# Performance work log

Hardware: AMD Instinct MI355X
Metric: run time of the kernel (lower is better)

Reference implementation:

```python
import jax, jax.numpy as jnp
import numpy as np

B, L, D = 8, 256, 256  # batch, max sentence length, channel_in == channel_out


def setup_inputs() -> dict:
    key = jax.random.key(0)
    k1, k2, k3, k4, k5, k6 = jax.random.split(key, 6)
    queries = jax.random.normal(k1, (B, L, D), dtype=jnp.float32)
    wordlens = jax.random.randint(k2, (B,), 1, L, dtype=jnp.int32)
    syntactic_dep = jax.random.randint(k3, (B, L, L), 0, 2, dtype=jnp.int32)
    # w_wc[0]: Linear(2D -> D, no bias); split its weight into the h_i and h_j halves.
    s1 = 1.0 / np.sqrt(2 * D)
    Wa = jax.random.normal(k4, (D, D), dtype=jnp.float32) * s1
    Wb = jax.random.normal(jax.random.fold_in(k4, 1), (D, D), dtype=jnp.float32) * s1
    # w_wc[3]: Linear(D -> 1, no bias)
    w2 = jax.random.normal(k5, (D,), dtype=jnp.float32) * (1.0 / np.sqrt(D))
    # wd: Linear(D -> D, no bias)
    Wd = jax.random.normal(k6, (D, D), dtype=jnp.float32) * (1.0 / np.sqrt(D))
    return {"queries": queries, "wordlens": wordlens, "syntactic_dep": syntactic_dep,
            "Wa": Wa, "Wb": Wb, "w2": w2, "Wd": Wd}


def reference(queries, wordlens, syntactic_dep, Wa, Wb, w2, Wd):
    # queries: [B, L, D]; syntactic_dep: [B, L, L] (nonzero => edge i->j)
    mask = syntactic_dep > 0
    # Edge score t_ij = w2 . relu(Wa h_i + Wb h_j)  (dropout is identity at eval)
    A = jnp.einsum('bid,cd->bic', queries, Wa)   # [B, L, C]
    Bm = jnp.einsum('bjd,cd->bjc', queries, Wb)  # [B, L, C]
    pre = jax.nn.relu(A[:, :, None, :] + Bm[:, None, :, :])  # [B, L, L, C]
    t = jnp.einsum('bijc,c->bij', pre, w2)       # [B, L, L]
    # T initialized to -100 everywhere, edge positions get t (exactly as original)
    T = jnp.where(mask, t, jnp.float32(-100.0))
    beta = jax.nn.softmax(T, axis=-1)            # softmax over j (dim=1 of [L, L])
    w = beta * mask.astype(beta.dtype)           # zero out non-edges after softmax
    hj = jnp.einsum('bjd,cd->bjc', queries, Wd)  # wd(h_j), [B, L, C]
    agg = jnp.einsum('bij,bjc->bic', w, hj)      # weighted neighbor sum
    output = jax.nn.relu(queries + agg)
    # skip=False, so no extra residual add
    return (output, wordlens, syntactic_dep)
```

## Files before the change

### kernel.cpp

```cpp
#include <hip/hip_runtime.h>

#define NB 8
#define LL 256
#define DD 256

typedef __attribute__((ext_vector_type(8))) short short8v;
typedef __attribute__((ext_vector_type(4))) float f32x4;

__device__ __forceinline__ uint f2bf2(float lo, float hi) {
  uint a = __float_as_uint(lo), b = __float_as_uint(hi);
  uint ra = (a + 0x7FFFu + ((a >> 16) & 1u)) >> 16;
  uint rb = (b + 0x7FFFu + ((b >> 16) & 1u)) & 0xFFFF0000u;
  return ra | rb;
}

__global__ __launch_bounds__(256) void gemm3_mfma(
    const float* __restrict__ Q, const float* __restrict__ Wa,
    const float* __restrict__ Wb, const float* __restrict__ Wd,
    float* __restrict__ A, float* __restrict__ Bm, float* __restrict__ Hj) {
  const int mt = blockIdx.x, nt = blockIdx.y, z = blockIdx.z;
  const float* __restrict__ W = (z == 0) ? Wa : (z == 1) ? Wb : Wd;
  float* __restrict__ Out = (z == 0) ? A : (z == 1) ? Bm : Hj;

  __shared__ __align__(16) ushort Qs[64][32];
  __shared__ __align__(16) ushort Ws[64][32];

  const int tid = threadIdx.x;
  const int m0 = mt * 64, n0 = nt * 64;
  const int srow = tid >> 2, skc = (tid & 3) * 8;
  const int w = tid >> 6, lane = tid & 63;
  const int wm = w >> 1, wn = w & 1;
  const int fr = lane & 15, fk = (lane >> 4) * 8;

  f32x4 acc[2][2] = {};
  for (int k0 = 0; k0 < DD; k0 += 32) {
    {
      const float* src = &Q[(size_t)(m0 + srow) * DD + k0 + skc];
      float4 q0 = *(const float4*)src;
      float4 q1 = *(const float4*)(src + 4);
      uint4 pk = make_uint4(f2bf2(q0.x, q0.y), f2bf2(q0.z, q0.w),
                            f2bf2(q1.x, q1.y), f2bf2(q1.z, q1.w));
      *(uint4*)&Qs[srow][skc] = pk;
      const float* ws_ = &W[(size_t)(n0 + srow) * DD + k0 + skc];
      float4 w0 = *(const float4*)ws_;
      float4 w1 = *(const float4*)(ws_ + 4);
      uint4 pw = make_uint4(f2bf2(w0.x, w0.y), f2bf2(w0.z, w0.w),
                            f2bf2(w1.x, w1.y), f2bf2(w1.z, w1.w));
      *(uint4*)&Ws[srow][skc] = pw;
    }
    __syncthreads();
    short8v a0 = *(const short8v*)&Qs[wm * 32 + fr][fk];
    short8v a1 = *(const short8v*)&Qs[wm * 32 + 16 + fr][fk];
    short8v b0 = *(const short8v*)&Ws[wn * 32 + fr][fk];
    short8v b1 = *(const short8v*)&Ws[wn * 32 + 16 + fr][fk];
    acc[0][0] = __builtin_amdgcn_mfma_f32_16x16x32_bf16(a0, b0, acc[0][0], 0, 0, 0);
    acc[0][1] = __builtin_amdgcn_mfma_f32_16x16x32_bf16(a0, b1, acc[0][1], 0, 0, 0);
    acc[1][0] = __builtin_amdgcn_mfma_f32_16x16x32_bf16(a1, b0, acc[1][0], 0, 0, 0);
    acc[1][1] = __builtin_amdgcn_mfma_f32_16x16x32_bf16(a1, b1, acc[1][1], 0, 0, 0);
    __syncthreads();
  }

  const int rbase = m0 + wm * 32 + (lane >> 4) * 4;
  const int cbase = n0 + wn * 32 + fr;
#pragma unroll
  for (int i = 0; i < 2; ++i)
#pragma unroll
    for (int j = 0; j < 2; ++j)
#pragma unroll
      for (int r = 0; r < 4; ++r)
        Out[(size_t)(rbase + i * 16 + r) * DD + cbase + j * 16] = acc[i][j][r];
}

__global__ __launch_bounds__(256) void fused_kernel(
    const float* __restrict__ Q, const int* __restrict__ sdep,
    const float* __restrict__ w2, const float* __restrict__ A,
    const float* __restrict__ Bm, const float* __restrict__ Hj,
    float* __restrict__ out, float* __restrict__ tail) {
  const int it = blockIdx.x, b = blockIdx.y;
  const int i0 = it * 4;
  const int tid = threadIdx.x;

  __shared__ float Ts[4][260];
  __shared__ float Red[4][4][256];

  {
    int base = (b * 64 + it) * 1024 + tid * 4;
    int4 s = *(const int4*)&sdep[base];
    float4 f;
    f.x = (float)s.x; f.y = (float)s.y; f.z = (float)s.z; f.w = (float)s.w;
    *(float4*)&tail[8 + base] = f;
  }

  const int w = tid >> 6, l = tid & 63;
  const int j0 = w * 64;

  {
    const int cg = l & 15;
    const int jp = l >> 4;
    float a[4][16], wv[16];
    const float* Ab = A + ((size_t)(b * LL + i0)) * DD + cg * 16;
#pragma unroll
    for (int r = 0; r < 4; ++r)
#pragma unroll
      for (int ch = 0; ch < 4; ++ch)
        *(float4*)&a[r][ch * 4] = *(const float4*)&Ab[(size_t)r * DD + ch * 4];
#pragma unroll
    for (int ch = 0; ch < 4; ++ch)
      *(float4*)&wv[ch * 4] = *(const float4*)&w2[cg * 16 + ch * 4];

    const float* Bb = Bm + ((size_t)(b * LL + j0 + jp)) * DD + cg * 16;
#pragma unroll 2
    for (int step = 0; step < 16; ++step) {
      float bv[16];
#pragma unroll
      for (int ch = 0; ch < 4; ++ch)
        *(float4*)&bv[ch * 4] =
            *(const float4*)&Bb[(size_t)step * 4 * DD + ch * 4];
      float p0 = 0.f, p1 = 0.f, p2 = 0.f, p3 = 0.f;
#pragma unroll
      for (int u = 0; u < 16; ++u) {
        float bb = bv[u], ww = wv[u];
        p0 = fmaf(ww, fmaxf(a[0][u] + bb, 0.f), p0);
        p1 = fmaf(ww, fmaxf(a[1][u] + bb, 0.f), p1);
        p2 = fmaf(ww, fmaxf(a[2][u] + bb, 0.f), p2);
        p3 = fmaf(ww, fmaxf(a[3][u] + bb, 0.f), p3);
      }
#pragma unroll
      for (int m = 1; m <= 8; m <<= 1) {
        p0 += __shfl_xor(p0, m);
        p1 += __shfl_xor(p1, m);
        p2 += __shfl_xor(p2, m);
        p3 += __shfl_xor(p3, m);
      }
      int j = j0 + step * 4 + jp;
      float pv = (cg == 0) ? p0 : (cg == 1) ? p1 : (cg == 2) ? p2 : p3;
      if (cg < 4) Ts[cg][j] = pv;
    }
  }
  __syncthreads();

  {
    const int* sr = sdep + ((size_t)(b * LL + i0 + w)) * LL;
    float v[4];
    float m = -3.0e38f;
#pragma unroll
    for (int k = 0; k < 4; ++k) {
      int j = l + 64 * k;
      bool e = sr[j] > 0;
      v[k] = e ? Ts[w][j] : -3.0e38f;
      m = fmaxf(m, v[k]);
    }
#pragma unroll
    for (int off = 32; off >= 1; off >>= 1) m = fmaxf(m, __shfl_xor(m, off));
    float s = 0.f;
#pragma unroll
    for (int k = 0; k < 4; ++k) {
      float e = (v[k] > -1.0e30f) ? __expf(v[k] - m) : 0.f;
      v[k] = e;
      s += e;
    }
#pragma unroll
    for (int off = 32; off >= 1; off >>= 1) s += __shfl_xor(s, off);
    float inv = (s > 0.f) ? 1.0f / s : 0.f;
    __syncthreads();
#pragma unroll
    for (int k = 0; k < 4; ++k) Ts[w][l + 64 * k] = v[k] * inv;
  }
  __syncthreads();

  {
    const float* Hb = Hj + ((size_t)(b * LL + j0)) * DD + l * 4;
    float acc[4][4] = {};
#pragma unroll 2
    for (int j4 = 0; j4 < 16; ++j4) {
      float tw0[4], tw1[4], tw2[4], tw3[4];
      *(float4*)tw0 = *(const float4*)&Ts[0][j0 + j4 * 4];
      *(float4*)tw1 = *(const float4*)&Ts[1][j0 + j4 * 4];
      *(float4*)tw2 = *(const float4*)&Ts[2][j0 + j4 * 4];
      *(float4*)tw3 = *(const float4*)&Ts[3][j0 + j4 * 4];
#pragma unroll
      for (int u = 0; u < 4; ++u) {
        float4 h = *(const float4*)&Hb[(size_t)(j4 * 4 + u) * DD];
        acc[0][0] = fmaf(tw0[u], h.x, acc[0][0]);
        acc[0][1] = fmaf(tw0[u], h.y, acc[0][1]);
        acc[0][2] = fmaf(tw0[u], h.z, acc[0][2]);
        acc[0][3] = fmaf(tw0[u], h.w, acc[0][3]);
        acc[1][0] = fmaf(tw1[u], h.x, acc[1][0]);
        acc[1][1] = fmaf(tw1[u], h.y, acc[1][1]);
        acc[1][2] = fmaf(tw1[u], h.z, acc[1][2]);
        acc[1][3] = fmaf(tw1[u], h.w, acc[1][3]);
        acc[2][0] = fmaf(tw2[u], h.x, acc[2][0]);
        acc[2][1] = fmaf(tw2[u], h.y, acc[2][1]);
        acc[2][2] = fmaf(tw2[u], h.z, acc[2][2]);
        acc[2][3] = fmaf(tw2[u], h.w, acc[2][3]);
        acc[3][0] = fmaf(tw3[u], h.x, acc[3][0]);
        acc[3][1] = fmaf(tw3[u], h.y, acc[3][1]);
        acc[3][2] = fmaf(tw3[u], h.z, acc[3][2]);
        acc[3][3] = fmaf(tw3[u], h.w, acc[3][3]);
      }
    }
#pragma unroll
    for (int r = 0; r < 4; ++r)
      *(float4*)&Red[w][r][l * 4] = *(float4*)acc[r];
  }
  __syncthreads();

  {
    const int r = tid >> 6, q = tid & 63;
    float4 s0 = *(const float4*)&Red[0][r][q * 4];
    float4 s1 = *(const float4*)&Red[1][r][q * 4];
    float4 s2 = *(const float4*)&Red[2][r][q * 4];
    float4 s3 = *(const float4*)&Red[3][r][q * 4];
    size_t off = ((size_t)(b * LL + i0 + r)) * DD + q * 4;
    float4 qv = *(const float4*)&Q[off];
    float4 o;
    o.x = fmaxf(qv.x + s0.x + s1.x + s2.x + s3.x, 0.f);
    o.y = fmaxf(qv.y + s0.y + s1.y + s2.y + s3.y, 0.f);
    o.z = fmaxf(qv.z + s0.z + s1.z + s2.z + s3.z, 0.f);
    o.w = fmaxf(qv.w + s0.w + s1.w + s2.w + s3.w, 0.f);
    *(float4*)&out[off] = o;
  }
}

__global__ void wordlen_kernel(const int* __restrict__ wl,
                               float* __restrict__ tail) {
  if (threadIdx.x < 8) tail[threadIdx.x] = (float)wl[threadIdx.x];
}

extern "C" void kernel_launch(void* const* d_in, const int* in_sizes, int n_in,
                              void* d_out, int out_size, void* d_ws, size_t ws_size,
                              hipStream_t stream) {
  const float* Q    = (const float*)d_in[0];
  const int*   wl   = (const int*)d_in[1];
  const int*   sdep = (const int*)d_in[2];
  const float* Wa   = (const float*)d_in[3];
  const float* Wb   = (const float*)d_in[4];
  const float* w2   = (const float*)d_in[5];
  const float* Wd   = (const float*)d_in[6];
  float* out = (float*)d_out;
  float* ws  = (float*)d_ws;

  float* A  = ws;
  float* Bm = ws + 524288;
  float* Hj = ws + 1048576;
  float* tail = out + (size_t)NB * LL * DD;

  wordlen_kernel<<<1, 64, 0, stream>>>(wl, tail);
  gemm3_mfma<<<dim3(32, 4, 3), 256, 0, stream>>>(Q, Wa, Wb, Wd, A, Bm, Hj);
  fused_kernel<<<dim3(64, 8), 256, 0, stream>>>(Q, sdep, w2, A, Bm, Hj,
                                                out, tail);
}
```

Measured before the change: 105.5 us.

## Move tail copies into GEMM kernel and widen fused blocks to eight rows

The sdep-to-float tail copy and the wordlen write now run inside the GEMM kernel, which removes one launch and takes that copy out of the fused kernel. The fused kernel now handles 8 query rows per 512-thread block with 8 waves, each covering 32 j columns, so each Bm row loaded is reused across twice as many rows. The number of fused blocks is halved to 256. The cost is higher register pressure from the a[8][16] array and a two-pass aggregation with extra barriers.

```diff
diff --git a/kernel.cpp b/kernel.cpp
--- a/kernel.cpp
+++ b/kernel.cpp
@@ -17,8 +17,11 @@
 __global__ __launch_bounds__(256) void gemm3_mfma(
     const float* __restrict__ Q, const float* __restrict__ Wa,
     const float* __restrict__ Wb, const float* __restrict__ Wd,
-    float* __restrict__ A, float* __restrict__ Bm, float* __restrict__ Hj) {
+    const int* __restrict__ wl, const int* __restrict__ sdep,
+    float* __restrict__ A, float* __restrict__ Bm, float* __restrict__ Hj,
+    float* __restrict__ tail) {
   const int mt = blockIdx.x, nt = blockIdx.y, z = blockIdx.z;
+  const int bid = mt + 32 * (nt + 4 * z);
   const float* __restrict__ W = (z == 0) ? Wa : (z == 1) ? Wb : Wd;
   float* __restrict__ Out = (z == 0) ? A : (z == 1) ? Bm : Hj;
 
@@ -69,38 +72,38 @@
 #pragma unroll
       for (int r = 0; r < 4; ++r)
         Out[(size_t)(rbase + i * 16 + r) * DD + cbase + j * 16] = acc[i][j][r];
-}
-
-__global__ __launch_bounds__(256) void fused_kernel(
+
+  for (int t = bid * 256 + tid; t < 131072; t += 384 * 256) {
+    int4 s = *(const int4*)&sdep[(size_t)t * 4];
+    float4 f;
+    f.x = (float)s.x; f.y = (float)s.y; f.z = (float)s.z; f.w = (float)s.w;
+    *(float4*)&tail[8 + (size_t)t * 4] = f;
+  }
+  if (bid == 0 && tid < 8) tail[tid] = (float)wl[tid];
+}
+
+__global__ __launch_bounds__(512, 2) void fused_kernel(
     const float* __restrict__ Q, const int* __restrict__ sdep,
     const float* __restrict__ w2, const float* __restrict__ A,
     const float* __restrict__ Bm, const float* __restrict__ Hj,
-    float* __restrict__ out, float* __restrict__ tail) {
-  const int it = blockIdx.x, b = blockIdx.y;
-  const int i0 = it * 4;
+    float* __restrict__ out) {
+  const int bid = blockIdx.x;
+  const int b = bid & 7, it = bid >> 3;
+  const int i0 = it * 8;
   const int tid = threadIdx.x;
-
-  __shared__ float Ts[4][260];
-  __shared__ float Red[4][4][256];
+  const int w = tid >> 6, l = tid & 63;
+  const int j0 = w * 32;
+
+  __shared__ float Ts[8][260];
+  __shared__ float Red[8][4][256];
 
   {
-    int base = (b * 64 + it) * 1024 + tid * 4;
-    int4 s = *(const int4*)&sdep[base];
-    float4 f;
-    f.x = (float)s.x; f.y = (float)s.y; f.z = (float)s.z; f.w = (float)s.w;
-    *(float4*)&tail[8 + base] = f;
-  }
-
-  const int w = tid >> 6, l = tid & 63;
-  const int j0 = w * 64;
-
-  {
+    const int jp = l >> 4;
     const int cg = l & 15;
-    const int jp = l >> 4;
-    float a[4][16], wv[16];
+    float a[8][16], wv[16];
     const float* Ab = A + ((size_t)(b * LL + i0)) * DD + cg * 16;
 #pragma unroll
-    for (int r = 0; r < 4; ++r)
+    for (int r = 0; r < 8; ++r)
 #pragma unroll
       for (int ch = 0; ch < 4; ++ch)
         *(float4*)&a[r][ch * 4] = *(const float4*)&Ab[(size_t)r * DD + ch * 4];
@@ -110,13 +113,14 @@
 
     const float* Bb = Bm + ((size_t)(b * LL + j0 + jp)) * DD + cg * 16;
 #pragma unroll 2
-    for (int step = 0; step < 16; ++step) {
+    for (int s = 0; s < 8; ++s) {
       float bv[16];
 #pragma unroll
       for (int ch = 0; ch < 4; ++ch)
         *(float4*)&bv[ch * 4] =
-            *(const float4*)&Bb[(size_t)step * 4 * DD + ch * 4];
+            *(const float4*)&Bb[(size_t)(s * 4) * DD + ch * 4];
       float p0 = 0.f, p1 = 0.f, p2 = 0.f, p3 = 0.f;
+      float p4 = 0.f, p5 = 0.f, p6 = 0.f, p7 = 0.f;
 #pragma unroll
       for (int u = 0; u < 16; ++u) {
         float bb = bv[u], ww = wv[u];
@@ -124,17 +128,24 @@
         p1 = fmaf(ww, fmaxf(a[1][u] + bb, 0.f), p1);
         p2 = fmaf(ww, fmaxf(a[2][u] + bb, 0.f), p2);
         p3 = fmaf(ww, fmaxf(a[3][u] + bb, 0.f), p3);
+        p4 = fmaf(ww, fmaxf(a[4][u] + bb, 0.f), p4);
+        p5 = fmaf(ww, fmaxf(a[5][u] + bb, 0.f), p5);
+        p6 = fmaf(ww, fmaxf(a[6][u] + bb, 0.f), p6);
+        p7 = fmaf(ww, fmaxf(a[7][u] + bb, 0.f), p7);
       }
 #pragma unroll
       for (int m = 1; m <= 8; m <<= 1) {
-        p0 += __shfl_xor(p0, m);
-        p1 += __shfl_xor(p1, m);
-        p2 += __shfl_xor(p2, m);
-        p3 += __shfl_xor(p3, m);
+        p0 += __shfl_xor(p0, m); p1 += __shfl_xor(p1, m);
+        p2 += __shfl_xor(p2, m); p3 += __shfl_xor(p3, m);
+        p4 += __shfl_xor(p4, m); p5 += __shfl_xor(p5, m);
+        p6 += __shfl_xor(p6, m); p7 += __shfl_xor(p7, m);
       }
-      int j = j0 + step * 4 + jp;
-      float pv = (cg == 0) ? p0 : (cg == 1) ? p1 : (cg == 2) ? p2 : p3;
-      if (cg < 4) Ts[cg][j] = pv;
+      float pv = p0;
+      pv = (cg == 1) ? p1 : pv; pv = (cg == 2) ? p2 : pv;
+      pv = (cg == 3) ? p3 : pv; pv = (cg == 4) ? p4 : pv;
+      pv = (cg == 5) ? p5 : pv; pv = (cg == 6) ? p6 : pv;
+      pv = (cg == 7) ? p7 : pv;
+      if (cg < 8) Ts[cg][j0 + s * 4 + jp] = pv;
     }
   }
   __syncthreads();
@@ -168,63 +179,69 @@
   }
   __syncthreads();
 
-  {
-    const float* Hb = Hj + ((size_t)(b * LL + j0)) * DD + l * 4;
-    float acc[4][4] = {};
+  const float* Hb = Hj + ((size_t)(b * LL + j0)) * DD + l * 4;
+#pragma unroll
+  for (int g = 0; g < 2; ++g) {
+    {
+      float acc[4][4] = {};
 #pragma unroll 2
-    for (int j4 = 0; j4 < 16; ++j4) {
-      float tw0[4], tw1[4], tw2[4], tw3[4];
-      *(float4*)tw0 = *(const float4*)&Ts[0][j0 + j4 * 4];
-      *(float4*)tw1 = *(const float4*)&Ts[1][j0 + j4 * 4];
-      *(float4*)tw2 = *(const float4*)&Ts[2][j0 + j4 * 4];
-      *(float4*)tw3 = *(const float4*)&Ts[3][j0 + j4 * 4];
-#pragma unroll
-      for (int u = 0; u < 4; ++u) {
-        float4 h = *(const float4*)&Hb[(size_t)(j4 * 4 + u) * DD];
-        acc[0][0] = fmaf(tw0[u], h.x, acc[0][0]);
-        acc[0][1] = fmaf(tw0[u], h.y, acc[0][1]);
-        acc[0][2] = fmaf(tw0[u], h.z, acc[0][2]);
-        acc[0][3] = fmaf(tw0[u], h.w, acc[0][3]);
-        acc[1][0] = fmaf(tw1[u], h.x, acc[1][0]);
-        acc[1][1] = fmaf(tw1[u], h.y, acc[1][1]);
-        acc[1][2] = fmaf(tw1[u], h.z, acc[1][2]);
-        acc[1][3] = fmaf(tw1[u], h.w, acc[1][3]);
-        acc[2][0] = fmaf(tw2[u], h.x, acc[2][0]);
-        acc[2][1] = fmaf(tw2[u], h.y, acc[2][1]);
-        acc[2][2] = fmaf(tw2[u], h.z, acc[2][2]);
-        acc[2][3] = fmaf(tw2[u], h.w, acc[2][3]);
-        acc[3][0] = fmaf(tw3[u], h.x, acc[3][0]);
-        acc[3][1] = fmaf(tw3[u], h.y, acc[3][1]);
-        acc[3][2] = fmaf(tw3[u], h.z, acc[3][2]);
-        acc[3][3] = fmaf(tw3[u], h.w, acc[3][3]);
+      for (int j4 = 0; j4 < 8; ++j4) {
+        float tw0[4], tw1[4], tw2[4], tw3[4];
+        *(float4*)tw0 = *(const float4*)&Ts[g * 4 + 0][j0 + j4 * 4];
+        *(float4*)tw1 = *(const float4*)&Ts[g * 4 + 1][j0 + j4 * 4];
+        *(float4*)tw2 = *(const float4*)&Ts[g * 4 + 2][j0 + j4 * 4];
+        *(float4*)tw3 = *(const float4*)&Ts[g * 4 + 3][j0 + j4 * 4];
+#pragma unroll
+        for (int u = 0; u < 4; ++u) {
+          float4 h = *(const float4*)&Hb[(size_t)(j4 * 4 + u) * DD];
+          acc[0][0] = fmaf(tw0[u], h.x, acc[0][0]);
+          acc[0][1] = fmaf(tw0[u], h.y, acc[0][1]);
+          acc[0][2] = fmaf(tw0[u], h.z, acc[0][2]);
+          acc[0][3] = fmaf(tw0[u], h.w, acc[0][3]);
+          acc[1][0] = fmaf(tw1[u], h.x, acc[1][0]);
+          acc[1][1] = fmaf(tw1[u], h.y, acc[1][1]);
+          acc[1][2] = fmaf(tw1[u], h.z, acc[1][2]);
+          acc[1][3] = fmaf(tw1[u], h.w, acc[1][3]);
+          acc[2][0] = fmaf(tw2[u], h.x, acc[2][0]);
+          acc[2][1] = fmaf(tw2[u], h.y, acc[2][1]);
+          acc[2][2] = fmaf(tw2[u], h.z, acc[2][2]);
+          acc[2][3] = fmaf(tw2[u], h.w, acc[2][3]);
+          acc[3][0] = fmaf(tw3[u], h.x, acc[3][0]);
+          acc[3][1] = fmaf(tw3[u], h.y, acc[3][1]);
+          acc[3][2] = fmaf(tw3[u], h.z, acc[3][2]);
+          acc[3][3] = fmaf(tw3[u], h.w, acc[3][3]);
+        }
       }
-    }
-#pragma unroll
-    for (int r = 0; r < 4; ++r)
-      *(float4*)&Red[w][r][l * 4] = *(float4*)acc[r];
-  }
-  __syncthreads();
-
-  {
-    const int r = tid >> 6, q = tid & 63;
-    float4 s0 = *(const float4*)&Red[0][r][q * 4];
-    float4 s1 = *(const float4*)&Red[1][r][q * 4];
-    float4 s2 = *(const float4*)&Red[2][r][q * 4];
-    float4 s3 = *(const float4*)&Red[3][r][q * 4];
-    size_t off = ((size_t)(b * LL + i0 + r)) * DD + q * 4;
-    float4 qv = *(const float4*)&Q[off];
-    float4 o;
-    o.x = fmaxf(qv.x + s0.x + s1.x + s2.x + s3.x, 0.f);
-    o.y = fmaxf(qv.y + s0.y + s1.y + s2.y + s3.y, 0.f);
-    o.z = fmaxf(qv.z + s0.z + s1.z + s2.z + s3.z, 0.f);
-    o.w = fmaxf(qv.w + s0.w + s1.w + s2.w + s3.w, 0.f);
-    *(float4*)&out[off] = o;
-  }
-}
-
-__global__ void wordlen_kernel(const int* __restrict__ wl,
-                               float* __restrict__ tail) {
-  if (threadIdx.x < 8) tail[threadIdx.x] = (float)wl[threadIdx.x];
+#pragma unroll
+      for (int r = 0; r < 4; ++r)
+        *(float4*)&Red[w][r][l * 4] = *(float4*)acc[r];
+    }
+    __syncthreads();
+    if (tid < 256) {
+      const int r = tid >> 6, q = tid & 63;
+      float4 s0 = *(const float4*)&Red[0][r][q * 4];
+      float4 s1 = *(const float4*)&Red[1][r][q * 4];
+      float4 s2 = *(const float4*)&Red[2][r][q * 4];
+      float4 s3 = *(const float4*)&Red[3][r][q * 4];
+      float4 s4 = *(const float4*)&Red[4][r][q * 4];
+      float4 s5 = *(const float4*)&Red[5][r][q * 4];
+      float4 s6 = *(const float4*)&Red[6][r][q * 4];
+      float4 s7 = *(const float4*)&Red[7][r][q * 4];
+      size_t off = ((size_t)(b * LL + i0 + g * 4 + r)) * DD + q * 4;
+      float4 qv = *(const float4*)&Q[off];
+      float4 o;
+      o.x = fmaxf(qv.x + ((s0.x + s1.x) + (s2.x + s3.x)) +
+                          ((s4.x + s5.x) + (s6.x + s7.x)), 0.f);
+      o.y = fmaxf(qv.y + ((s0.y + s1.y) + (s2.y + s3.y)) +
+                          ((s4.y + s5.y) + (s6.y + s7.y)), 0.f);
+      o.z = fmaxf(qv.z + ((s0.z + s1.z) + (s2.z + s3.z)) +
+                          ((s4.z + s5.z) + (s6.z + s7.z)), 0.f);
+      o.w = fmaxf(qv.w + ((s0.w + s1.w) + (s2.w + s3.w)) +
+                          ((s4.w + s5.w) + (s6.w + s7.w)), 0.f);
+      *(float4*)&out[off] = o;
+    }
+    __syncthreads();
+  }
 }
 
 extern "C" void kernel_launch(void* const* d_in, const int* in_sizes, int n_in,
@@ -245,8 +262,7 @@
   float* Hj = ws + 1048576;
   float* tail = out + (size_t)NB * LL * DD;
 
-  wordlen_kernel<<<1, 64, 0, stream>>>(wl, tail);
-  gemm3_mfma<<<dim3(32, 4, 3), 256, 0, stream>>>(Q, Wa, Wb, Wd, A, Bm, Hj);
-  fused_kernel<<<dim3(64, 8), 256, 0, stream>>>(Q, sdep, w2, A, Bm, Hj,
-                                                out, tail);
-}
+  gemm3_mfma<<<dim3(32, 4, 3), 256, 0, stream>>>(Q, Wa, Wb, Wd, wl, sdep,
+                                                 A, Bm, Hj, tail);
+  fused_kernel<<<256, 512, 0, stream>>>(Q, sdep, w2, A, Bm, Hj, out);
+}
```

Result: faster. 102.9 us (-2.5%).
